# Performance work log

Measured on AMD Instinct MI355X. Metric: run time of the kernel, lower is better.

Reference implementation:

```python
import jax, jax.numpy as jnp
import numpy as np

EPS = 1e-8  # torch F.cosine_similarity norm clamp


def _l2norm(x):
    # normalize along last axis with torch-style eps clamp
    nrm = jnp.sqrt(jnp.sum(x * x, axis=-1))
    return x / jnp.maximum(nrm, EPS)[..., None]


def setup_inputs() -> dict:
    key = jax.random.key(0)
    k1, k2 = jax.random.split(key)
    n, c, h, w = 32, 64, 192, 192
    output = jax.random.normal(k1, (n, c, h, w), dtype=jnp.float32)
    target = jax.random.normal(k2, (n, c, h, w), dtype=jnp.float32)
    return {"output": output, "target": target}


def reference(output, target):
    n, c, h, w = output.shape
    # torch: output_h, _ = output.max(dim=-1)  -> values over width, shape (n,c,h)
    out_h = jnp.max(output, axis=-1)   # (n,c,h)
    out_w = jnp.max(output, axis=-2)   # (n,c,w)
    tgt_h = jnp.max(target, axis=-1)
    tgt_w = jnp.max(target, axis=-2)

    Po_h = jax.nn.softmax(out_h, axis=2)
    Pt_h = jax.nn.softmax(tgt_h, axis=2)
    Po_w = jax.nn.softmax(out_w, axis=2)
    Pt_w = jax.nn.softmax(tgt_w, axis=2)

    # normalize once; cosine sim = dot of unit vectors
    Ao_h, At_h = _l2norm(Po_h), _l2norm(Pt_h)
    Ao_w, At_w = _l2norm(Po_w), _l2norm(Pt_w)

    # positive (matched-channel) similarity, shape (n,c)
    h_sim_pos = jnp.sum(Ao_h * At_h, axis=2)
    w_sim_pos = jnp.sum(Ao_w * At_w, axis=2)
    sim_pos = 0.5 * (h_sim_pos + w_sim_pos)

    # full pairwise sum over all (i,j) channel pairs -> shape (n,)
    sim_h = jnp.einsum('nik,njk->n', Ao_h, At_h)
    sim_w = jnp.einsum('nik,njk->n', Ao_w, At_w)
    sim = 0.5 * (sim_h + sim_w)

    loss = -jnp.log(sim_pos / sim[:, None])  # (n,c)
    loss = loss / c / n
    return loss
```

## Files before the change

### kernel.cpp

```cpp
#include <hip/hip_runtime.h>
#include <math.h>

#define N_  32
#define C_  64
#define HW  192
#define NC  (N_ * C_)

__device__ __forceinline__ float wave_max(float v) {
#pragma unroll
    for (int off = 32; off; off >>= 1) v = fmaxf(v, __shfl_xor(v, off));
    return v;
}
__device__ __forceinline__ float wave_sum(float v) {
#pragma unroll
    for (int off = 32; off; off >>= 1) v += __shfl_xor(v, off);
    return v;
}

__device__ __forceinline__ float block_max(float v, float* red) {
    const int w = threadIdx.x >> 6, lane = threadIdx.x & 63;
    v = wave_max(v);
    if (lane == 0) red[w] = v;
    __syncthreads();
    float r = fmaxf(fmaxf(red[0], red[1]), fmaxf(red[2], red[3]));
    __syncthreads();
    return r;
}
__device__ __forceinline__ float block_sum(float v, float* red) {
    const int w = threadIdx.x >> 6, lane = threadIdx.x & 63;
    v = wave_sum(v);
    if (lane == 0) red[w] = v;
    __syncthreads();
    float r = (red[0] + red[1]) + (red[2] + red[3]);
    __syncthreads();
    return r;
}

__global__ void k_zero(float* __restrict__ S, int n) {
    int i = blockIdx.x * blockDim.x + threadIdx.x;
    if (i < n) S[i] = 0.0f;
}

__global__ __launch_bounds__(256) void k_stage1(const float* __restrict__ outp,
                                                const float* __restrict__ tgtp,
                                                float* __restrict__ simpos,
                                                float* __restrict__ S) {
    __shared__ float rowmax[HW];
    __shared__ float colpart[4][HW];
    __shared__ float colmax[HW];
    __shared__ float A[4][HW];
    __shared__ float red[4];

    const int b    = blockIdx.x;
    const int n    = b >> 6;
    const int tid  = threadIdx.x;
    const int w    = tid >> 6;
    const int lane = tid & 63;
    const float NEG = -INFINITY;

    for (int t = 0; t < 2; ++t) {
        const float* X = (t == 0 ? outp : tgtp) + (size_t)b * (HW * HW);

        float4 colp = make_float4(NEG, NEG, NEG, NEG);
        for (int r = w; r < HW; r += 4) {
            float rm = NEG;
            if (lane < 48) {
                const float4 v = ((const float4*)(X + r * HW))[lane];
                colp.x = fmaxf(colp.x, v.x);
                colp.y = fmaxf(colp.y, v.y);
                colp.z = fmaxf(colp.z, v.z);
                colp.w = fmaxf(colp.w, v.w);
                rm = fmaxf(fmaxf(v.x, v.y), fmaxf(v.z, v.w));
            }
            rm = wave_max(rm);
            if (lane == 0) rowmax[r] = rm;
        }
        if (lane < 48) {
            colpart[w][4 * lane + 0] = colp.x;
            colpart[w][4 * lane + 1] = colp.y;
            colpart[w][4 * lane + 2] = colp.z;
            colpart[w][4 * lane + 3] = colp.w;
        }
        __syncthreads();
        if (tid < HW) {
            colmax[tid] = fmaxf(fmaxf(colpart[0][tid], colpart[1][tid]),
                                fmaxf(colpart[2][tid], colpart[3][tid]));
        }
        __syncthreads();

        for (int vsel = 0; vsel < 2; ++vsel) {
            const float* src = (vsel == 0) ? rowmax : colmax;
            float x = (tid < HW) ? src[tid] : NEG;
            float M = block_max(x, red);
            float e = (tid < HW) ? expf(x - M) : 0.0f;
            float ss = block_sum(e * e, red);
            if (tid < HW) A[t * 2 + vsel][tid] = e / sqrtf(ss);
        }
        __syncthreads();
    }

    float p = 0.0f;
    if (tid < HW) p = A[0][tid] * A[2][tid] + A[1][tid] * A[3][tid];
    float sp = block_sum(p, red);
    if (tid == 0) simpos[b] = 0.5f * sp;

    if (tid < HW) {
        float* Sn = S + (size_t)n * 4 * HW;
        atomicAdd(Sn + 0 * HW + tid, A[0][tid]);
        atomicAdd(Sn + 1 * HW + tid, A[2][tid]);
        atomicAdd(Sn + 2 * HW + tid, A[1][tid]);
        atomicAdd(Sn + 3 * HW + tid, A[3][tid]);
    }
}

__global__ __launch_bounds__(256) void k_stage2(const float* __restrict__ simpos,
                                                const float* __restrict__ S,
                                                float* __restrict__ loss) {
    __shared__ float red[4];
    const int n = blockIdx.x, tid = threadIdx.x;
    const float* Sn = S + (size_t)n * 4 * HW;
    float p = 0.0f;
    if (tid < HW)
        p = Sn[tid] * Sn[HW + tid] + Sn[2 * HW + tid] * Sn[3 * HW + tid];
    float sim = 0.5f * block_sum(p, red);
    if (tid < C_) {
        loss[n * C_ + tid] =
            -logf(simpos[n * C_ + tid] / sim) * (1.0f / (N_ * C_));
    }
}

extern "C" void kernel_launch(void* const* d_in, const int* in_sizes, int n_in,
                              void* d_out, int out_size, void* d_ws, size_t ws_size,
                              hipStream_t stream) {
    const float* outp = (const float*)d_in[0];
    const float* tgtp = (const float*)d_in[1];
    float* simpos = (float*)d_ws;
    float* S      = simpos + NC;
    float* lossp  = (float*)d_out;

    const int s_elems = N_ * 4 * HW;
    hipLaunchKernelGGL(k_zero, dim3((s_elems + 255) / 256), dim3(256), 0, stream,
                       S, s_elems);
    hipLaunchKernelGGL(k_stage1, dim3(NC), dim3(256), 0, stream,
                       outp, tgtp, simpos, S);
    hipLaunchKernelGGL(k_stage2, dim3(N_), dim3(256), 0, stream,
                       simpos, S, lossp);
}
```

Measured before the change: 571.4 us.

## Load both tensors per row with 12 float4 loads in flight, drop atomics

The stage-1 kernel now reads rows of both output and target together, each thread loading 12 float4 values at once, so more memory requests are outstanding per thread and the all-lane 48-of-64 mask is gone. Column maxima are merged through a padded shared-memory buffer. The global atomicAdd accumulation and the zeroing kernel are replaced by writing per-channel normalized vectors to workspace, which stage 2 then sums per batch. This adds workspace traffic and a serial 64-iteration loop in stage 2 in exchange for removing atomics and one launch.

```diff
diff --git a/kernel.cpp b/kernel.cpp
--- a/kernel.cpp
+++ b/kernel.cpp
@@ -36,93 +36,124 @@
     return r;
 }
 
-__global__ void k_zero(float* __restrict__ S, int n) {
-    int i = blockIdx.x * blockDim.x + threadIdx.x;
-    if (i < n) S[i] = 0.0f;
-}
+#define FMAX4(a, v)                                                    \
+    do {                                                               \
+        (a).x = fmaxf((a).x, (v).x); (a).y = fmaxf((a).y, (v).y);      \
+        (a).z = fmaxf((a).z, (v).z); (a).w = fmaxf((a).w, (v).w);      \
+    } while (0)
 
 __global__ __launch_bounds__(256) void k_stage1(const float* __restrict__ outp,
                                                 const float* __restrict__ tgtp,
                                                 float* __restrict__ simpos,
-                                                float* __restrict__ S) {
-    __shared__ float rowmax[HW];
-    __shared__ float colpart[4][HW];
-    __shared__ float colmax[HW];
+                                                float* __restrict__ Aout) {
+    __shared__ float4 cpart[32][49];
+    __shared__ float rowm[2][HW];
+    __shared__ float colm[2][HW];
     __shared__ float A[4][HW];
     __shared__ float red[4];
 
-    const int b    = blockIdx.x;
-    const int n    = b >> 6;
-    const int tid  = threadIdx.x;
-    const int w    = tid >> 6;
-    const int lane = tid & 63;
+    const int b   = blockIdx.x;
+    const int tid = threadIdx.x;
+    const int j   = tid & 7;
+    const int r   = tid >> 3;
     const float NEG = -INFINITY;
 
+    const float* X0 = outp + (size_t)b * (HW * HW);
+    const float* X1 = tgtp + (size_t)b * (HW * HW);
+
+    float4 cm0[6], cm1[6];
+#pragma unroll
+    for (int k = 0; k < 6; ++k) {
+        cm0[k] = make_float4(NEG, NEG, NEG, NEG);
+        cm1[k] = cm0[k];
+    }
+
+    for (int p = 0; p < 6; ++p) {
+        const int row = p * 32 + r;
+        const float4* r0 = (const float4*)(X0 + row * HW);
+        const float4* r1 = (const float4*)(X1 + row * HW);
+        float4 v0[6], v1[6];
+#pragma unroll
+        for (int k = 0; k < 6; ++k) v0[k] = r0[j + 8 * k];
+#pragma unroll
+        for (int k = 0; k < 6; ++k) v1[k] = r1[j + 8 * k];
+
+        float rm0 = NEG, rm1 = NEG;
+#pragma unroll
+        for (int k = 0; k < 6; ++k) {
+            FMAX4(cm0[k], v0[k]);
+            FMAX4(cm1[k], v1[k]);
+            rm0 = fmaxf(rm0, fmaxf(fmaxf(v0[k].x, v0[k].y), fmaxf(v0[k].z, v0[k].w)));
+            rm1 = fmaxf(rm1, fmaxf(fmaxf(v1[k].x, v1[k].y), fmaxf(v1[k].z, v1[k].w)));
+        }
+#pragma unroll
+        for (int off = 1; off < 8; off <<= 1) {
+            rm0 = fmaxf(rm0, __shfl_xor(rm0, off));
+            rm1 = fmaxf(rm1, __shfl_xor(rm1, off));
+        }
+        if (j == 0) { rowm[0][row] = rm0; rowm[1][row] = rm1; }
+    }
+
     for (int t = 0; t < 2; ++t) {
-        const float* X = (t == 0 ? outp : tgtp) + (size_t)b * (HW * HW);
-
-        float4 colp = make_float4(NEG, NEG, NEG, NEG);
-        for (int r = w; r < HW; r += 4) {
-            float rm = NEG;
-            if (lane < 48) {
-                const float4 v = ((const float4*)(X + r * HW))[lane];
-                colp.x = fmaxf(colp.x, v.x);
-                colp.y = fmaxf(colp.y, v.y);
-                colp.z = fmaxf(colp.z, v.z);
-                colp.w = fmaxf(colp.w, v.w);
-                rm = fmaxf(fmaxf(v.x, v.y), fmaxf(v.z, v.w));
-            }
-            rm = wave_max(rm);
-            if (lane == 0) rowmax[r] = rm;
-        }
-        if (lane < 48) {
-            colpart[w][4 * lane + 0] = colp.x;
-            colpart[w][4 * lane + 1] = colp.y;
-            colpart[w][4 * lane + 2] = colp.z;
-            colpart[w][4 * lane + 3] = colp.w;
-        }
+        __syncthreads();
+#pragma unroll
+        for (int k = 0; k < 6; ++k) cpart[r][j + 8 * k] = t ? cm1[k] : cm0[k];
         __syncthreads();
         if (tid < HW) {
-            colmax[tid] = fmaxf(fmaxf(colpart[0][tid], colpart[1][tid]),
-                                fmaxf(colpart[2][tid], colpart[3][tid]));
+            const int c4 = tid >> 2, comp = tid & 3;
+            float m = NEG;
+#pragma unroll 4
+            for (int rr = 0; rr < 32; ++rr) {
+                m = fmaxf(m, ((const float*)&cpart[rr][c4])[comp]);
+            }
+            colm[t][tid] = m;
         }
-        __syncthreads();
+    }
+    __syncthreads();
 
-        for (int vsel = 0; vsel < 2; ++vsel) {
-            const float* src = (vsel == 0) ? rowmax : colmax;
-            float x = (tid < HW) ? src[tid] : NEG;
-            float M = block_max(x, red);
-            float e = (tid < HW) ? expf(x - M) : 0.0f;
-            float ss = block_sum(e * e, red);
-            if (tid < HW) A[t * 2 + vsel][tid] = e / sqrtf(ss);
-        }
-        __syncthreads();
+    for (int v = 0; v < 4; ++v) {
+        const float* src = (v == 0) ? rowm[0] : (v == 1) ? colm[0]
+                         : (v == 2) ? rowm[1] : colm[1];
+        float x = (tid < HW) ? src[tid] : NEG;
+        float M = block_max(x, red);
+        float e = (tid < HW) ? expf(x - M) : 0.0f;
+        float ss = block_sum(e * e, red);
+        if (tid < HW) A[v][tid] = e / sqrtf(ss);
     }
+    __syncthreads();
 
-    float p = 0.0f;
-    if (tid < HW) p = A[0][tid] * A[2][tid] + A[1][tid] * A[3][tid];
-    float sp = block_sum(p, red);
+    float pd = (tid < HW) ? (A[0][tid] * A[2][tid] + A[1][tid] * A[3][tid]) : 0.0f;
+    float sp = block_sum(pd, red);
     if (tid == 0) simpos[b] = 0.5f * sp;
 
-    if (tid < HW) {
-        float* Sn = S + (size_t)n * 4 * HW;
-        atomicAdd(Sn + 0 * HW + tid, A[0][tid]);
-        atomicAdd(Sn + 1 * HW + tid, A[2][tid]);
-        atomicAdd(Sn + 2 * HW + tid, A[1][tid]);
-        atomicAdd(Sn + 3 * HW + tid, A[3][tid]);
-    }
+    float* dst = Aout + (size_t)b * 4 * HW;
+    const float* Af = (const float*)A;
+    for (int i = tid; i < 4 * HW; i += 256) dst[i] = Af[i];
 }
 
 __global__ __launch_bounds__(256) void k_stage2(const float* __restrict__ simpos,
-                                                const float* __restrict__ S,
+                                                const float* __restrict__ Aout,
                                                 float* __restrict__ loss) {
+    __shared__ float S[4 * HW];
     __shared__ float red[4];
     const int n = blockIdx.x, tid = threadIdx.x;
-    const float* Sn = S + (size_t)n * 4 * HW;
+    const float* base = Aout + (size_t)n * C_ * 4 * HW;
+
+    float a0 = 0.0f, a1 = 0.0f, a2 = 0.0f;
+    for (int c = 0; c < C_; ++c) {
+        const float* a = base + c * 4 * HW;
+        a0 += a[tid];
+        a1 += a[tid + 256];
+        a2 += a[tid + 512];
+    }
+    S[tid] = a0; S[tid + 256] = a1; S[tid + 512] = a2;
+    __syncthreads();
+
     float p = 0.0f;
     if (tid < HW)
-        p = Sn[tid] * Sn[HW + tid] + Sn[2 * HW + tid] * Sn[3 * HW + tid];
+        p = S[0 * HW + tid] * S[2 * HW + tid] + S[1 * HW + tid] * S[3 * HW + tid];
     float sim = 0.5f * block_sum(p, red);
+
     if (tid < C_) {
         loss[n * C_ + tid] =
             -logf(simpos[n * C_ + tid] / sim) * (1.0f / (N_ * C_));
@@ -135,14 +166,11 @@
     const float* outp = (const float*)d_in[0];
     const float* tgtp = (const float*)d_in[1];
     float* simpos = (float*)d_ws;
-    float* S      = simpos + NC;
+    float* Aout   = simpos + NC;
     float* lossp  = (float*)d_out;
 
-    const int s_elems = N_ * 4 * HW;
-    hipLaunchKernelGGL(k_zero, dim3((s_elems + 255) / 256), dim3(256), 0, stream,
-                       S, s_elems);
     hipLaunchKernelGGL(k_stage1, dim3(NC), dim3(256), 0, stream,
-                       outp, tgtp, simpos, S);
+                       outp, tgtp, simpos, Aout);
     hipLaunchKernelGGL(k_stage2, dim3(N_), dim3(256), 0, stream,
-                       simpos, S, lossp);
+                       simpos, Aout, lossp);
 }
```

Result: no change. 576.4 us (+0.9%).
